# Optimization experiments

Measured on AMD Instinct MI355X. Metric: run time of the kernel, lower is better.

## Reference

```python
import jax, jax.numpy as jnp
import numpy as np

N_HEAD = 8
D_HEAD = 64  # emb_size == d_model // n_head


def _proj(x, w):
    # x: (B, 1, d_model, max_len), w: (n_head*emb_size, 1, 25, 1) -> conv VALID
    y = jax.lax.conv_general_dilated(
        x, w, window_strides=(1, 1), padding='VALID',
        dimension_numbers=('NCHW', 'OIHW', 'NCHW'))  # (B, C, H1, L)
    B, C, H1, L = y.shape
    y = y.reshape(B, C, H1 // N_HEAD, N_HEAD, L).mean(axis=3)  # (B, C, H2, L)
    # view(B, -1, n_head, d_head).transpose(1, 2) -> (B, n_head, S, d_head)
    y = y.reshape(B, -1, N_HEAD, D_HEAD).transpose(0, 2, 1, 3)
    return y


def setup_inputs() -> dict:
    key = jax.random.key(0)
    ks = jax.random.split(key, 7)
    B, d_model, max_len = 8, 512, 16
    C = N_HEAD * D_HEAD  # 512
    return {
        'query': jax.random.normal(ks[0], (B, 1, d_model, max_len), jnp.float32),
        'key':   jax.random.normal(ks[1], (B, 1, d_model, max_len), jnp.float32),
        'value': jax.random.normal(ks[2], (B, 1, d_model, max_len), jnp.float32),
        'wq': jax.random.normal(ks[3], (C, 1, 25, 1), jnp.float32) * 0.1,
        'wk': jax.random.normal(ks[4], (C, 1, 25, 1), jnp.float32) * 0.1,
        'wv': jax.random.normal(ks[5], (C, 1, 25, 1), jnp.float32) * 0.1,
        'w_out': jax.random.normal(ks[6], (1, 1, 1, 1), jnp.float32),
        'b_out': jnp.zeros((1,), jnp.float32),
    }


def reference(query, key, value, wq, wk, wv, w_out, b_out):
    q = _proj(query, wq)   # (B, H, S, Dh)
    k = _proj(key, wk)
    v = _proj(value, wv)
    scale = 1.0 / jnp.sqrt(jnp.asarray(D_HEAD, q.dtype))
    scores = jnp.einsum('bhqd,bhkd->bhqk', q, k) * scale
    attn = jax.nn.softmax(scores, axis=-1)  # dropout is identity in eval
    x = jnp.einsum('bhqk,bhkd->bhqd', attn, v)
    B = x.shape[0]
    x = x.transpose(0, 2, 1, 3).reshape(B, -1, N_HEAD * D_HEAD)  # (B, S, d_model)
    # conv_out: 1x1 Conv2d(1,1) == scalar scale + bias
    x = x * w_out.reshape(()) + b_out.reshape(())
    return x, attn
```

## Files before the change

kernel.cpp:

```cpp
#include <hip/hip_runtime.h>
#include <hip/hip_bf16.h>
#include <cstdint>
#include <cstddef>

#define B_    8
#define H_    8
#define BH_   64
#define S_    976
#define SP_   992
#define D_    64
#define DM_   512
#define L_    16
#define H2_   61
#define KW_   25
#define EFF_  32
#define XOFF  3997696
#define OSTR  68
#define PWC   132

typedef __attribute__((ext_vector_type(8))) short bf16x8;
typedef __attribute__((ext_vector_type(4))) short bf16x4;
typedef __attribute__((ext_vector_type(4))) float f32x4;

__device__ __forceinline__ unsigned short f2bfu(float f) {
    union { float f; unsigned u; } v; v.f = f;
    unsigned u = v.u;
    u += 0x7fffu + ((u >> 16) & 1u);
    return (unsigned short)(u >> 16);
}
__device__ __forceinline__ unsigned packbf(float a, float b) {
    return (unsigned)f2bfu(a) | ((unsigned)f2bfu(b) << 16);
}
__device__ __forceinline__ float bflo(unsigned u) {
    union { unsigned u; float f; } v; v.u = u << 16; return v.f;
}
__device__ __forceinline__ float bfhi(unsigned u) {
    union { unsigned u; float f; } v; v.u = u & 0xffff0000u; return v.f;
}

__device__ __forceinline__ f32x4 mfma16(bf16x4 a, bf16x4 b, f32x4 c) {
#if __has_builtin(__builtin_amdgcn_mfma_f32_16x16x16bf16_1k)
    return __builtin_amdgcn_mfma_f32_16x16x16bf16_1k(a, b, c, 0, 0, 0);
#else
    asm volatile("v_mfma_f32_16x16x16_bf16 %0, %1, %2, %0"
                 : "+v"(c) : "v"(a), "v"(b));
    return c;
#endif
}

__global__ __launch_bounds__(256) void proj_kernel(
    const float* __restrict__ qin, const float* __restrict__ kin,
    const float* __restrict__ vin, const float* __restrict__ wq,
    const float* __restrict__ wk, const float* __restrict__ wv,
    short* __restrict__ qws, short* __restrict__ kws, short* __restrict__ vtws) {
    __shared__ float xl[536 * L_];
    __shared__ float wl[32 * 32];
    int blk = blockIdx.x;
    int cg  = blk & 15;
    int b   = (blk >> 4) & 7;
    int tz  = blk >> 7;
    const float* x    = (tz == 0) ? qin : (tz == 1) ? kin : vin;
    const float* wsrc = (tz == 0) ? wq  : (tz == 1) ? wk  : wv;

    const float4* xb4 = (const float4*)(x + b * DM_ * L_);
    float4* xl4 = (float4*)xl;
    for (int i = threadIdx.x; i < DM_ * L_ / 4; i += 256) xl4[i] = xb4[i];
    for (int i = DM_ * L_ + threadIdx.x; i < 536 * L_; i += 256) xl[i] = 0.f;

    for (int i = threadIdx.x; i < 1024; i += 256) {
        int ci = i >> 5;
        int t  = i & 31;
        int c  = cg * 32 + ci;
        int jlo = (t - 24 > 0) ? t - 24 : 0;
        int jhi = (t < 7) ? t : 7;
        float s = 0.f;
        for (int jj = jlo; jj <= jhi; ++jj) s += wsrc[c * KW_ + (t - jj)];
        wl[i] = s * 0.125f;
    }
    __syncthreads();

    int c_local = threadIdx.x >> 3;
    int plane   = threadIdx.x & 7;
    int c       = cg * 32 + c_local;
    float wreg[EFF_];
    #pragma unroll
    for (int i = 0; i < EFF_; ++i) wreg[i] = wl[c_local * 32 + i];

    for (int m = 0; m < 32; ++m) {
        int pg  = plane + 8 * m;
        int h2b = pg >> 4;
        int l   = pg & 15;
        float acc[4] = {0.f, 0.f, 0.f, 0.f};
        #pragma unroll
        for (int k = 0; k < 56; ++k) {
            float xv = xl[(h2b * 32 + k) * L_ + l];
            #pragma unroll
            for (int d = 0; d < 4; ++d) {
                int t = k - 8 * d;
                if (t >= 0 && t < EFF_) acc[d] = fmaf(xv, wreg[t], acc[d]);
            }
        }
        #pragma unroll
        for (int d = 0; d < 4; ++d) {
            int h2 = h2b * 4 + d;
            if (h2 < H2_) {
                int f    = c * S_ + h2 * L_ + l;
                int s    = f >> 9;
                int head = (f >> 6) & 7;
                int dh   = f & 63;
                int bh   = b * H_ + head;
                short bv = (short)f2bfu(acc[d]);
                if (tz == 0)      qws[((size_t)bh * S_ + s) * D_ + dh] = bv;
                else if (tz == 1) kws[((size_t)bh * S_ + s) * D_ + dh] = bv;
                else              vtws[((size_t)bh * D_ + dh) * SP_ + s] = bv;
            }
        }
    }
}

__global__ __launch_bounds__(256) void attn_kernel(
    const short* __restrict__ qws, const short* __restrict__ kws,
    const short* __restrict__ vtws, const float* __restrict__ w_out,
    const float* __restrict__ b_out, float* __restrict__ out) {
    __shared__ unsigned pw[4][16][PWC];
    __shared__ float sums[4][16];

    int w    = threadIdx.x >> 6;
    int lane = threadIdx.x & 63;
    int l16  = lane & 15;
    int g    = lane >> 4;

    int blk = blockIdx.x;
    int xcd = blk & 7;
    int j   = blk >> 3;
    int bh  = xcd + 8 * (j / H2_);
    int qt  = j % H2_;
    int s0  = qt * 16;

    int t0 = (w == 0) ? 0 : 16 + (w - 1) * 15;
    int nt = (w == 0) ? 16 : 15;

    const short* qb = qws + ((size_t)bh * S_ + s0 + l16) * D_ + g * 8;
    bf16x8 q0 = *(const bf16x8*)qb;
    bf16x8 q1 = *(const bf16x8*)(qb + 32);
    const short* kbase = kws + ((size_t)bh * S_ + l16) * D_ + g * 8;
    const short* vbase = vtws + ((size_t)bh * D_ + l16) * SP_ + g * 4;

    f32x4 o0 = {0.f,0.f,0.f,0.f}, o1 = {0.f,0.f,0.f,0.f};
    f32x4 o2 = {0.f,0.f,0.f,0.f}, o3 = {0.f,0.f,0.f,0.f};
    float sa = 0.f, sb = 0.f, sc_ = 0.f, sd = 0.f;

    bf16x8 nk0, nk1;
    bf16x4 nv0, nv1, nv2, nv3;
    {
        const short* kb = kbase + (size_t)t0 * 16 * D_;
        nk0 = *(const bf16x8*)kb;
        nk1 = *(const bf16x8*)(kb + 32);
        const short* vb = vbase + t0 * 16;
        nv0 = *(const bf16x4*)(vb);
        nv1 = *(const bf16x4*)(vb + 16 * SP_);
        nv2 = *(const bf16x4*)(vb + 32 * SP_);
        nv3 = *(const bf16x4*)(vb + 48 * SP_);
    }

    #pragma unroll
    for (int ct = 0; ct < 16; ++ct) {
        if (ct < nt) {
            bf16x8 k0 = nk0, k1 = nk1;
            bf16x4 v0 = nv0, v1 = nv1, v2 = nv2, v3 = nv3;
            if (ct + 1 < nt) {
                int gt = t0 + ct + 1;
                const short* kb = kbase + (size_t)gt * 16 * D_;
                nk0 = *(const bf16x8*)kb;
                nk1 = *(const bf16x8*)(kb + 32);
                const short* vb = vbase + gt * 16;
                nv0 = *(const bf16x4*)(vb);
                nv1 = *(const bf16x4*)(vb + 16 * SP_);
                nv2 = *(const bf16x4*)(vb + 32 * SP_);
                nv3 = *(const bf16x4*)(vb + 48 * SP_);
            }
            f32x4 acc = {0.f, 0.f, 0.f, 0.f};
            acc = __builtin_amdgcn_mfma_f32_16x16x32_bf16(k0, q0, acc, 0, 0, 0);
            acc = __builtin_amdgcn_mfma_f32_16x16x32_bf16(k1, q1, acc, 0, 0, 0);
            float e0 = __expf(acc[0] * 0.125f);
            float e1 = __expf(acc[1] * 0.125f);
            float e2 = __expf(acc[2] * 0.125f);
            float e3 = __expf(acc[3] * 0.125f);
            sa += e0; sb += e1; sc_ += e2; sd += e3;
            unsigned u0 = packbf(e0, e1);
            unsigned u1 = packbf(e2, e3);
            uint2 pk2 = {u0, u1};
            *(uint2*)(void*)&pw[w][l16][ct * 8 + g * 2] = pk2;
            union { uint2 u; bf16x4 v; } pc;
            pc.u.x = u0; pc.u.y = u1;
            o0 = mfma16(pc.v, v0, o0);
            o1 = mfma16(pc.v, v1, o1);
            o2 = mfma16(pc.v, v2, o2);
            o3 = mfma16(pc.v, v3, o3);
        }
    }
    float sum = (sa + sb) + (sc_ + sd);
    sum += __shfl_xor(sum, 16);
    sum += __shfl_xor(sum, 32);
    if (lane < 16) sums[w][l16] = sum;
    __syncthreads();

    {
        int colbase = t0 * 16;
        int ncol_u  = nt * 8;
        bool act = (lane * 2) < ncol_u;
        float* abase = out + XOFF + ((size_t)bh * S_ + s0) * S_ + colbase + lane * 4;
        #pragma unroll
        for (int r = 0; r < 16; ++r) {
            float invr = 1.f / ((sums[0][r] + sums[1][r]) +
                                (sums[2][r] + sums[3][r]));
            if (act) {
                uint2 raw = *(const uint2*)(void*)&pw[w][r][lane * 2];
                f32x4 pv = { bflo(raw.x) * invr, bfhi(raw.x) * invr,
                             bflo(raw.y) * invr, bfhi(raw.y) * invr };
                *(f32x4*)(abase + (size_t)r * S_) = pv;
            }
        }
    }
    __syncthreads();

    float* olds = (float*)&pw[0][0][0];
    if (w != 3) {
        float* ob = olds + w * 16 * OSTR;
        #pragma unroll
        for (int i = 0; i < 4; ++i) {
            int q = g * 4 + i;
            ob[q * OSTR +  0 + l16] = o0[i];
            ob[q * OSTR + 16 + l16] = o1[i];
            ob[q * OSTR + 32 + l16] = o2[i];
            ob[q * OSTR + 48 + l16] = o3[i];
        }
    }
    __syncthreads();

    if (w == 3) {
        float wo = w_out[0], bo = b_out[0];
        int b = bh >> 3, hh = bh & 7;
        #pragma unroll
        for (int i = 0; i < 4; ++i) {
            int q = g * 4 + i;
            float invq = 1.f / ((sums[0][q] + sums[1][q]) +
                                (sums[2][q] + sums[3][q]));
            float s1 = invq * wo;
            float* xr = out + ((size_t)b * S_ + s0 + q) * DM_ + hh * D_ + l16;
            int o = q * OSTR + l16;
            xr[0]  = (o0[i] + olds[o +  0] + olds[16*OSTR + o +  0] + olds[32*OSTR + o +  0]) * s1 + bo;
            xr[16] = (o1[i] + olds[o + 16] + olds[16*OSTR + o + 16] + olds[32*OSTR + o + 16]) * s1 + bo;
            xr[32] = (o2[i] + olds[o + 32] + olds[16*OSTR + o + 32] + olds[32*OSTR + o + 32]) * s1 + bo;
            xr[48] = (o3[i] + olds[o + 48] + olds[16*OSTR + o + 48] + olds[32*OSTR + o + 48]) * s1 + bo;
        }
    }
}

extern "C" void kernel_launch(void* const* d_in, const int* in_sizes, int n_in,
                              void* d_out, int out_size, void* d_ws, size_t ws_size,
                              hipStream_t stream) {
    const float* q   = (const float*)d_in[0];
    const float* k   = (const float*)d_in[1];
    const float* v   = (const float*)d_in[2];
    const float* wq  = (const float*)d_in[3];
    const float* wk  = (const float*)d_in[4];
    const float* wv  = (const float*)d_in[5];
    const float* wo  = (const float*)d_in[6];
    const float* bo  = (const float*)d_in[7];

    char* ws = (char*)d_ws;
    short* qws  = (short*)(ws + 196608);
    short* kws  = qws + (size_t)BH_ * S_ * D_;
    short* vtws = kws + (size_t)BH_ * S_ * D_;

    proj_kernel<<<384, 256, 0, stream>>>(q, k, v, wq, wk, wv, qws, kws, vtws);
    attn_kernel<<<BH_ * H2_, 256, 0, stream>>>(qws, kws, vtws, wo, bo,
                                               (float*)d_out);
}
```

Measured before the change: 165.8 us.

## Vectorize projection loads/stores, drop K/V prefetch, nontemporal attn stores, spread reduction

The projection kernel now gives each thread four adjacent L columns, reading float4 from LDS and writing Q/K as 4-wide bf16 vectors. This cuts LDS load count and the number of global stores. In the attention kernel the manual software prefetch of K/V is removed in favour of direct per-tile loads, leaving latency hiding to the compiler and scheduler. The attention-probability stores become nontemporal. The final output reduction is now spread across all four waves with coalesced 64-wide row stores, instead of being done by one wave.

```diff
diff --git a/kernel.cpp b/kernel.cpp
--- a/kernel.cpp
+++ b/kernel.cpp
@@ -20,6 +20,7 @@
 
 typedef __attribute__((ext_vector_type(8))) short bf16x8;
 typedef __attribute__((ext_vector_type(4))) short bf16x4;
+typedef __attribute__((ext_vector_type(4))) unsigned short u16x4;
 typedef __attribute__((ext_vector_type(4))) float f32x4;
 
 __device__ __forceinline__ unsigned short f2bfu(float f) {
@@ -80,39 +81,56 @@
     __syncthreads();
 
     int c_local = threadIdx.x >> 3;
-    int plane   = threadIdx.x & 7;
+    int slot    = threadIdx.x & 7;
     int c       = cg * 32 + c_local;
     float wreg[EFF_];
     #pragma unroll
     for (int i = 0; i < EFF_; ++i) wreg[i] = wl[c_local * 32 + i];
 
-    for (int m = 0; m < 32; ++m) {
-        int pg  = plane + 8 * m;
-        int h2b = pg >> 4;
-        int l   = pg & 15;
-        float acc[4] = {0.f, 0.f, 0.f, 0.f};
+    for (int it = 0; it < 8; ++it) {
+        int pt  = slot + it * 8;
+        int h2b = pt >> 2;
+        int l0  = (pt & 3) * 4;
+        float acc[4][4];
+        #pragma unroll
+        for (int d = 0; d < 4; ++d)
+            #pragma unroll
+            for (int jj = 0; jj < 4; ++jj) acc[d][jj] = 0.f;
+        const float* xp = &xl[(h2b * 32) * L_ + l0];
         #pragma unroll
         for (int k = 0; k < 56; ++k) {
-            float xv = xl[(h2b * 32 + k) * L_ + l];
+            float4 xv = *(const float4*)(xp + k * L_);
             #pragma unroll
             for (int d = 0; d < 4; ++d) {
                 int t = k - 8 * d;
-                if (t >= 0 && t < EFF_) acc[d] = fmaf(xv, wreg[t], acc[d]);
+                if (t >= 0 && t < EFF_) {
+                    acc[d][0] = fmaf(xv.x, wreg[t], acc[d][0]);
+                    acc[d][1] = fmaf(xv.y, wreg[t], acc[d][1]);
+                    acc[d][2] = fmaf(xv.z, wreg[t], acc[d][2]);
+                    acc[d][3] = fmaf(xv.w, wreg[t], acc[d][3]);
+                }
             }
         }
         #pragma unroll
         for (int d = 0; d < 4; ++d) {
             int h2 = h2b * 4 + d;
             if (h2 < H2_) {
-                int f    = c * S_ + h2 * L_ + l;
-                int s    = f >> 9;
-                int head = (f >> 6) & 7;
-                int dh   = f & 63;
+                int f0   = c * S_ + h2 * L_ + l0;
+                int s    = f0 >> 9;
+                int head = (f0 >> 6) & 7;
+                int dh   = f0 & 63;
                 int bh   = b * H_ + head;
-                short bv = (short)f2bfu(acc[d]);
-                if (tz == 0)      qws[((size_t)bh * S_ + s) * D_ + dh] = bv;
-                else if (tz == 1) kws[((size_t)bh * S_ + s) * D_ + dh] = bv;
-                else              vtws[((size_t)bh * D_ + dh) * SP_ + s] = bv;
+                if (tz == 2) {
+                    #pragma unroll
+                    for (int jj = 0; jj < 4; ++jj)
+                        vtws[((size_t)bh * D_ + dh + jj) * SP_ + s] =
+                            (short)f2bfu(acc[d][jj]);
+                } else {
+                    u16x4 u = { f2bfu(acc[d][0]), f2bfu(acc[d][1]),
+                                f2bfu(acc[d][2]), f2bfu(acc[d][3]) };
+                    short* dst = (tz == 0) ? qws : kws;
+                    *(u16x4*)(void*)&dst[((size_t)bh * S_ + s) * D_ + dh] = u;
+                }
             }
         }
     }
@@ -150,35 +168,18 @@
     f32x4 o2 = {0.f,0.f,0.f,0.f}, o3 = {0.f,0.f,0.f,0.f};
     float sa = 0.f, sb = 0.f, sc_ = 0.f, sd = 0.f;
 
-    bf16x8 nk0, nk1;
-    bf16x4 nv0, nv1, nv2, nv3;
-    {
-        const short* kb = kbase + (size_t)t0 * 16 * D_;
-        nk0 = *(const bf16x8*)kb;
-        nk1 = *(const bf16x8*)(kb + 32);
-        const short* vb = vbase + t0 * 16;
-        nv0 = *(const bf16x4*)(vb);
-        nv1 = *(const bf16x4*)(vb + 16 * SP_);
-        nv2 = *(const bf16x4*)(vb + 32 * SP_);
-        nv3 = *(const bf16x4*)(vb + 48 * SP_);
-    }
-
     #pragma unroll
     for (int ct = 0; ct < 16; ++ct) {
         if (ct < nt) {
-            bf16x8 k0 = nk0, k1 = nk1;
-            bf16x4 v0 = nv0, v1 = nv1, v2 = nv2, v3 = nv3;
-            if (ct + 1 < nt) {
-                int gt = t0 + ct + 1;
-                const short* kb = kbase + (size_t)gt * 16 * D_;
-                nk0 = *(const bf16x8*)kb;
-                nk1 = *(const bf16x8*)(kb + 32);
-                const short* vb = vbase + gt * 16;
-                nv0 = *(const bf16x4*)(vb);
-                nv1 = *(const bf16x4*)(vb + 16 * SP_);
-                nv2 = *(const bf16x4*)(vb + 32 * SP_);
-                nv3 = *(const bf16x4*)(vb + 48 * SP_);
-            }
+            int gt = t0 + ct;
+            const short* kb = kbase + (size_t)gt * 16 * D_;
+            bf16x8 k0 = *(const bf16x8*)kb;
+            bf16x8 k1 = *(const bf16x8*)(kb + 32);
+            const short* vb = vbase + gt * 16;
+            bf16x4 v0 = *(const bf16x4*)(vb);
+            bf16x4 v1 = *(const bf16x4*)(vb + 16 * SP_);
+            bf16x4 v2 = *(const bf16x4*)(vb + 32 * SP_);
+            bf16x4 v3 = *(const bf16x4*)(vb + 48 * SP_);
             f32x4 acc = {0.f, 0.f, 0.f, 0.f};
             acc = __builtin_amdgcn_mfma_f32_16x16x32_bf16(k0, q0, acc, 0, 0, 0);
             acc = __builtin_amdgcn_mfma_f32_16x16x32_bf16(k1, q1, acc, 0, 0, 0);
@@ -207,8 +208,7 @@
 
     {
         int colbase = t0 * 16;
-        int ncol_u  = nt * 8;
-        bool act = (lane * 2) < ncol_u;
+        bool act = lane < nt * 4;
         float* abase = out + XOFF + ((size_t)bh * S_ + s0) * S_ + colbase + lane * 4;
         #pragma unroll
         for (int r = 0; r < 16; ++r) {
@@ -218,14 +218,14 @@
                 uint2 raw = *(const uint2*)(void*)&pw[w][r][lane * 2];
                 f32x4 pv = { bflo(raw.x) * invr, bfhi(raw.x) * invr,
                              bflo(raw.y) * invr, bfhi(raw.y) * invr };
-                *(f32x4*)(abase + (size_t)r * S_) = pv;
+                __builtin_nontemporal_store(pv, (f32x4*)(abase + (size_t)r * S_));
             }
         }
     }
     __syncthreads();
 
     float* olds = (float*)&pw[0][0][0];
-    if (w != 3) {
+    {
         float* ob = olds + w * 16 * OSTR;
         #pragma unroll
         for (int i = 0; i < 4; ++i) {
@@ -238,21 +238,19 @@
     }
     __syncthreads();
 
-    if (w == 3) {
+    {
         float wo = w_out[0], bo = b_out[0];
         int b = bh >> 3, hh = bh & 7;
         #pragma unroll
-        for (int i = 0; i < 4; ++i) {
-            int q = g * 4 + i;
-            float invq = 1.f / ((sums[0][q] + sums[1][q]) +
-                                (sums[2][q] + sums[3][q]));
-            float s1 = invq * wo;
-            float* xr = out + ((size_t)b * S_ + s0 + q) * DM_ + hh * D_ + l16;
-            int o = q * OSTR + l16;
-            xr[0]  = (o0[i] + olds[o +  0] + olds[16*OSTR + o +  0] + olds[32*OSTR + o +  0]) * s1 + bo;
-            xr[16] = (o1[i] + olds[o + 16] + olds[16*OSTR + o + 16] + olds[32*OSTR + o + 16]) * s1 + bo;
-            xr[32] = (o2[i] + olds[o + 32] + olds[16*OSTR + o + 32] + olds[32*OSTR + o + 32]) * s1 + bo;
-            xr[48] = (o3[i] + olds[o + 48] + olds[16*OSTR + o + 48] + olds[32*OSTR + o + 48]) * s1 + bo;
+        for (int rr = 0; rr < 4; ++rr) {
+            int r = w * 4 + rr;
+            float invr = 1.f / ((sums[0][r] + sums[1][r]) +
+                                (sums[2][r] + sums[3][r]));
+            float s1 = invr * wo;
+            int o = r * OSTR + lane;
+            float v = olds[o] + olds[16*OSTR + o] + olds[32*OSTR + o] +
+                      olds[48*OSTR + o];
+            out[((size_t)b * S_ + s0 + r) * DM_ + hh * D_ + lane] = v * s1 + bo;
         }
     }
 }
```

Result: slower. 176.3 us (+6.3%).
